# Performance work log

Measured on AMD Instinct MI355X. Metric: run time of the kernel, lower is better.

The kernel has to match this reference:

```python
import jax, jax.numpy as jnp
import numpy as np

S, B, TD = 1024, 2, 138
D, H, Dh, L, F = 1024, 16, 64, 8, 2048
EPS = 1e-5


def setup_inputs() -> dict:
    key = jax.random.key(0)
    ks = jax.random.split(key, 32)
    std = 0.02

    def w(k, shape):
        return (jax.random.normal(k, shape, jnp.float32) * std)

    return {
        'tokens': jax.random.normal(ks[0], (S, B, TD), jnp.float32),
        'Win': w(ks[1], (D, TD)), 'bin_': jnp.zeros((D,), jnp.float32),
        'pos_emb': w(ks[2], (S, D)),
        'Wq': w(ks[3], (L, D, D)), 'bq': jnp.zeros((L, D), jnp.float32),
        'Wk': w(ks[4], (L, D, D)), 'bk': jnp.zeros((L, D), jnp.float32),
        'Wv': w(ks[5], (L, D, D)), 'bv': jnp.zeros((L, D), jnp.float32),
        'Wo': w(ks[6], (L, D, D)), 'bo': jnp.zeros((L, D), jnp.float32),
        'W1': w(ks[7], (L, F, D)), 'b1': jnp.zeros((L, F), jnp.float32),
        'W2': w(ks[8], (L, D, F)), 'b2': jnp.zeros((L, D), jnp.float32),
        'g1': jnp.ones((L, D), jnp.float32), 'be1': jnp.zeros((L, D), jnp.float32),
        'g2': jnp.ones((L, D), jnp.float32), 'be2': jnp.zeros((L, D), jnp.float32),
        'Wh': w(ks[9], (1, D)), 'bh': jnp.zeros((1,), jnp.float32),
    }


def _ln(x, g, b):
    mu = jnp.mean(x, axis=-1, keepdims=True)
    var = jnp.mean(jnp.square(x - mu), axis=-1, keepdims=True)
    return (x - mu) * jax.lax.rsqrt(var + EPS) * g + b


def _rope_tables(seq_len):
    inv_freq = 1.0 / (10000.0 ** (jnp.arange(0, Dh, 2, dtype=jnp.float32) / Dh))
    ang = jnp.arange(seq_len, dtype=jnp.float32)[:, None] * inv_freq  # (S, Dh/2)
    cos = jnp.repeat(jnp.cos(ang), 2, axis=-1)  # (S, Dh) interleaved
    sin = jnp.repeat(jnp.sin(ang), 2, axis=-1)
    return cos, sin


def _apply_rope(x, cos, sin):
    # x: (B, H, S, Dh); rotate_every_two: pairs (x0, x1) -> (-x1, x0)
    rot = jnp.stack([-x[..., 1::2], x[..., 0::2]], axis=-1).reshape(x.shape)
    return x * cos + rot * sin


def reference(tokens, Win, bin_, pos_emb, Wq, bq, Wk, bk, Wv, bv, Wo, bo,
              W1, b1, W2, b2, g1, be1, g2, be2, Wh, bh):
    s = tokens.shape[0]
    x = jnp.einsum('sbt,dt->sbd', tokens, Win) + bin_ + pos_emb[:s, None, :]
    cos, sin = _rope_tables(s)
    causal = jnp.tril(jnp.ones((s, s), dtype=bool))
    scale = 1.0 / np.sqrt(Dh)

    def to_heads(y):  # (S,B,D) -> (B,H,S,Dh)
        return jnp.transpose(y.reshape(s, -1, H, Dh), (1, 2, 0, 3))

    def layer(x, p):
        wq, bq_, wk, bk_, wv, bv_, wo, bo_, w1, b1_, w2, b2_, g1_, be1_, g2_, be2_ = p
        qh = _apply_rope(to_heads(jnp.einsum('sbd,ed->sbe', x, wq) + bq_), cos, sin)
        kh = _apply_rope(to_heads(jnp.einsum('sbd,ed->sbe', x, wk) + bk_), cos, sin)
        vh = to_heads(jnp.einsum('sbd,ed->sbe', x, wv) + bv_)
        scores = jnp.einsum('bhqd,bhkd->bhqk', qh, kh) * scale
        scores = jnp.where(causal, scores, -jnp.inf)
        attn = jax.nn.softmax(scores, axis=-1)
        o = jnp.einsum('bhqk,bhkd->bhqd', attn, vh)  # (B,H,S,Dh)
        o = jnp.transpose(o, (2, 0, 1, 3)).reshape(s, -1, D)
        attn_out = jnp.einsum('sbd,ed->sbe', o, wo) + bo_
        src2 = _ln(x + attn_out, g1_, be1_)
        ff = jnp.einsum('sbf,df->sbd', jax.nn.relu(jnp.einsum('sbd,fd->sbf', src2, w1) + b1_), w2) + b2_
        return _ln(src2 + ff, g2_, be2_), None

    params = (Wq, bq, Wk, bk, Wv, bv, Wo, bo, W1, b1, W2, b2, g1, be1, g2, be2)
    x, _ = jax.lax.scan(layer, x, params)
    return jnp.einsum('sbd,od->sbo', x, Wh) + bh  # (S, B, 1)
```

## Files before the change

### kernel.cpp

```cpp
#include <hip/hip_runtime.h>
#include <hip/hip_bf16.h>

typedef __hip_bfloat16 bf16;
typedef float f32x4 __attribute__((ext_vector_type(4)));
typedef float f32x16 __attribute__((ext_vector_type(16)));
typedef short s16x8 __attribute__((ext_vector_type(8)));
typedef int i32x4 __attribute__((ext_vector_type(4)));

#define S_LEN 1024
#define BATCH 2
#define TDIM 138
#define KPAD 160
#define DMOD 1024
#define NHEAD 16
#define DHEAD 64
#define NLAYER 8
#define FDIM 2048
#define MROWS 2048
static const size_t DD_ = (size_t)DMOD * DMOD;
static const size_t FD_ = (size_t)FDIM * DMOD;

__device__ __forceinline__ void load_lds16(const bf16* g, bf16* l) {
  __builtin_amdgcn_global_load_lds((const __attribute__((address_space(1))) void*)g,
                                   (__attribute__((address_space(3))) void*)l, 16, 0, 0);
}

__device__ __forceinline__ unsigned pack2(float a, float b) {
  unsigned x = __builtin_bit_cast(unsigned short, __float2bfloat16(a));
  unsigned y = __builtin_bit_cast(unsigned short, __float2bfloat16(b));
  return x | (y << 16);
}

__device__ __forceinline__ int chunk_start(int c) {
  return c == 0 ? 0 : (c == 1 ? 32 : (c == 2 ? 56 : 72));
}

__global__ __launch_bounds__(256) void f2b_layer(
    const float4* __restrict__ Wq, const float4* __restrict__ Wk,
    const float4* __restrict__ Wv, const float4* __restrict__ Wo,
    const float4* __restrict__ W1, const float4* __restrict__ W2,
    ushort4* __restrict__ dst) {
  int i = blockIdx.x * 256 + threadIdx.x;
  const int DD4 = (int)(DD_ / 4), FD4 = (int)(FD_ / 4);
  if (i >= 4 * DD4 + 2 * FD4) return;
  const float4* src; int off;
  if (i < 3 * DD4) { int w = i / DD4; off = i - w * DD4; src = w == 0 ? Wq : (w == 1 ? Wk : Wv); }
  else if (i < 4 * DD4) { src = Wo; off = i - 3 * DD4; }
  else if (i < 4 * DD4 + FD4) { src = W1; off = i - 4 * DD4; }
  else { src = W2; off = i - 4 * DD4 - FD4; }
  float4 v = src[off];
  ushort4 o;
  o.x = __builtin_bit_cast(unsigned short, __float2bfloat16(v.x));
  o.y = __builtin_bit_cast(unsigned short, __float2bfloat16(v.y));
  o.z = __builtin_bit_cast(unsigned short, __float2bfloat16(v.z));
  o.w = __builtin_bit_cast(unsigned short, __float2bfloat16(v.w));
  dst[i] = o;
}

__global__ __launch_bounds__(256) void pad_cvt(const float* __restrict__ in,
                                               bf16* __restrict__ out, int R) {
  int i = blockIdx.x * 256 + threadIdx.x;
  if (i >= R * KPAD) return;
  int r = i / KPAD, t = i - r * KPAD;
  out[i] = __float2bfloat16(t < TDIM ? in[r * TDIM + t] : 0.0f);
}

__global__ __launch_bounds__(256) void rope_table(float2* __restrict__ t) {
  int idx = blockIdx.x * 256 + threadIdx.x;
  if (idx >= S_LEN * 32) return;
  int s = idx >> 5, i = idx & 31;
  float freq = __expf(-(float)i * (2.0f / (float)DHEAD) * 9.210340371976184f);
  float sn, cs;
  sincosf((float)s * freq, &sn, &cs);
  t[idx] = make_float2(cs, sn);
}

template<int TN, int EPI>
__global__ __launch_bounds__(512) void gemm128(
    const bf16* __restrict__ A, const bf16* __restrict__ W,
    const float* __restrict__ b0p, const float* __restrict__ b1p, const float* __restrict__ b2p,
    const float2* __restrict__ rope2, float* __restrict__ Cf,
    bf16* __restrict__ Cb0, bf16* __restrict__ Cb1, bf16* __restrict__ Cb2,
    int N, int K, int nbx) {
  constexpr int NJ = TN / 32;
  constexpr int ASZ = 128 * 32, BSZ = TN * 32;
  __shared__ bf16 As[4 * ASZ];
  __shared__ bf16 Bs[4 * BSZ];
  int nwg = gridDim.x, bid = blockIdx.x;
  int wg = (bid & 7) * (nwg >> 3) + (bid >> 3);
  int bx = wg % nbx, by = wg / nbx;
  int bn = bx * TN, bm = by * 128;
  int tid = threadIdx.x, lane = tid & 63, w = tid >> 6;
  int lo = lane & 15, hi = lane >> 4;
  int wr = (w >> 1) * 32, wc = (w & 1) * (TN / 2);
  f32x4 acc[2][NJ] = {};

  int srow = tid >> 2, sseg = tid & 3;
  int srb = (tid & 255) >> 2;
  const bf16* gA = A + (size_t)(bm + srow) * K + sseg * 8;
  const bf16* gB = W + (size_t)(bn + (TN == 128 ? srow : srb)) * K + sseg * 8;
  bf16* lA0 = As + srow * 32 + sseg * 8;
  bf16* lB0 = Bs + (TN == 128 ? srow : srb) * 32 + sseg * 8;

  auto STAGE = [&](int k0, int b) {
    load_lds16(gA + k0, lA0 + b * ASZ);
    if constexpr (TN == 128) {
      load_lds16(gB + k0, lB0 + b * BSZ);
    } else {
      if (tid < 256) load_lds16(gB + k0, lB0 + b * BSZ);
    }
  };

  int nt = K / 32;
  STAGE(0, 0);
  STAGE(32, 1);
  STAGE(64, 2);

  for (int t = 0; t < nt; t++) {
    int rem = nt - 1 - t;
    if constexpr (TN == 128) {
      if (rem >= 2)      asm volatile("s_waitcnt vmcnt(4)" ::: "memory");
      else if (rem == 1) asm volatile("s_waitcnt vmcnt(2)" ::: "memory");
      else               asm volatile("s_waitcnt vmcnt(0)" ::: "memory");
    } else {
      if (tid < 256) {
        if (rem >= 2)      asm volatile("s_waitcnt vmcnt(4)" ::: "memory");
        else if (rem == 1) asm volatile("s_waitcnt vmcnt(2)" ::: "memory");
        else               asm volatile("s_waitcnt vmcnt(0)" ::: "memory");
      } else {
        if (rem >= 2)      asm volatile("s_waitcnt vmcnt(2)" ::: "memory");
        else if (rem == 1) asm volatile("s_waitcnt vmcnt(1)" ::: "memory");
        else               asm volatile("s_waitcnt vmcnt(0)" ::: "memory");
      }
    }
    __builtin_amdgcn_s_barrier();
    __builtin_amdgcn_sched_barrier(0);

    const bf16* Ab = As + (t & 3) * ASZ;
    const bf16* Bb = Bs + (t & 3) * BSZ;
    s16x8 af[2], bfr[NJ];
#pragma unroll
    for (int mi = 0; mi < 2; mi++) af[mi] = *(const s16x8*)(Ab + (wr + mi * 16 + lo) * 32 + hi * 8);
#pragma unroll
    for (int nj = 0; nj < NJ; nj++) bfr[nj] = *(const s16x8*)(Bb + (wc + nj * 16 + lo) * 32 + hi * 8);
#pragma unroll
    for (int mi = 0; mi < 2; mi++)
#pragma unroll
      for (int nj = 0; nj < NJ; nj++)
        acc[mi][nj] = __builtin_amdgcn_mfma_f32_16x16x32_bf16(af[mi], bfr[nj], acc[mi][nj], 0, 0, 0);

    __builtin_amdgcn_sched_barrier(0);
    __builtin_amdgcn_s_barrier();
    __builtin_amdgcn_sched_barrier(0);
    if (t + 3 < nt) STAGE((t + 3) * 32, (t + 3) & 3);
  }

#pragma unroll
  for (int mi = 0; mi < 2; mi++)
#pragma unroll
    for (int nj = 0; nj < NJ; nj++)
#pragma unroll
      for (int r = 0; r < 4; r++) {
        int m = bm + wr + mi * 16 + hi * 4 + r;
        int n = bn + wc + nj * 16 + lo;
        float v = acc[mi][nj][r];
        if constexpr (EPI == 0) {
          int which = n >> 10;
          int d = n & 1023, h = d >> 6, dh = d & 63;
          int s = m >> 1, bb = m & 1;
          const float* bp = which == 0 ? b0p : (which == 1 ? b1p : b2p);
          v += bp[d];
          if (which < 2) {
            float pv = __shfl_xor(v, 1);
            float2 cn = rope2[s * 32 + (dh >> 1)];
            float o = (dh & 1) ? (v * cn.x + pv * cn.y) : (v * cn.x - pv * cn.y);
            bf16* dst = which == 0 ? Cb0 : Cb1;
            dst[(((size_t)(bb * NHEAD + h)) * S_LEN + s) * DHEAD + dh] = __float2bfloat16(o);
          } else {
            Cb2[(((size_t)(bb * NHEAD + h)) * DHEAD + dh) * S_LEN + s] = __float2bfloat16(v);
          }
        } else if constexpr (EPI == 1) {
          Cf[(size_t)m * N + n] = v + b0p[n];
        } else if constexpr (EPI == 2) {
          Cb0[(size_t)m * N + n] = __float2bfloat16(fmaxf(v + b0p[n], 0.0f));
        } else {
          float v2 = v + b0p[n] + b1p[(size_t)(m >> 1) * DMOD + n];
          Cf[(size_t)m * N + n] = v2;
          Cb0[(size_t)m * N + n] = __float2bfloat16(v2);
        }
      }
}

__global__ __launch_bounds__(256) void flash_part(const bf16* __restrict__ Q,
    const bf16* __restrict__ K, const bf16* __restrict__ Vt,
    float* __restrict__ pO, float* __restrict__ pML) {
  int bid = blockIdx.x;
  int xcd = bid & 7, idx = bid >> 3;
  int bh = xcd * 4 + idx / 20;
  int w = threadIdx.x >> 6, lane = threadIdx.x & 63;
  int widx = (idx % 20) * 4 + w;
  int c = widx < 32 ? 0 : (widx < 56 ? 1 : (widx < 72 ? 2 : 3));
  int qt = widx - chunk_start(c) + 8 * c;
  int l31 = lane & 31, hi1 = lane >> 5;
  int q0 = qt * 32, kc0 = c * 256;
  int kend = min(kc0 + 256, q0 + 32);
  int nkt = (kend - kc0 + 31) >> 5;

  const size_t qkb = (size_t)bh * S_LEN * DHEAD;
  const bf16* qp = Q + qkb + (size_t)(q0 + l31) * DHEAD + hi1 * 8;
  s16x8 bq0 = *(const s16x8*)(qp);
  s16x8 bq1 = *(const s16x8*)(qp + 16);
  s16x8 bq2 = *(const s16x8*)(qp + 32);
  s16x8 bq3 = *(const s16x8*)(qp + 48);
  const bf16* kB = K + qkb;
  const bf16* vB = Vt + qkb;
  f32x16 accO0 = {}, accO1 = {};
  float mv = -INFINITY, lv = 0.0f;
  const float SC = 0.18033688011112042f;

  auto loadTile = [&](int kc, s16x8& k0, s16x8& k1, s16x8& k2, s16x8& k3,
                      s16x8& v0, s16x8& v1, s16x8& v2, s16x8& v3) {
    const bf16* kp = kB + (size_t)(kc + l31) * DHEAD + hi1 * 8;
    k0 = *(const s16x8*)(kp);
    k1 = *(const s16x8*)(kp + 16);
    k2 = *(const s16x8*)(kp + 32);
    k3 = *(const s16x8*)(kp + 48);
    const bf16* vp = vB + (size_t)l31 * S_LEN + kc + hi1 * 8;
    v0 = *(const s16x8*)(vp);
    v1 = *(const s16x8*)(vp + 16);
    v2 = *(const s16x8*)(vp + (size_t)32 * S_LEN);
    v3 = *(const s16x8*)(vp + (size_t)32 * S_LEN + 16);
  };

  auto computeTile = [&](int kc, s16x8 ka0, s16x8 ka1, s16x8 ka2, s16x8 ka3,
                         s16x8 va00, s16x8 va01, s16x8 va10, s16x8 va11) {
    f32x16 st = {};
    st = __builtin_amdgcn_mfma_f32_32x32x16_bf16(ka0, bq0, st, 0, 0, 0);
    st = __builtin_amdgcn_mfma_f32_32x32x16_bf16(ka1, bq1, st, 0, 0, 0);
    st = __builtin_amdgcn_mfma_f32_32x32x16_bf16(ka2, bq2, st, 0, 0, 0);
    st = __builtin_amdgcn_mfma_f32_32x32x16_bf16(ka3, bq3, st, 0, 0, 0);

    bool diag = (kc >= q0);
    float pmax = -INFINITY;
#pragma unroll
    for (int j = 0; j < 16; j++) {
      float s = st[j] * SC;
      if (diag) {
        int krow = kc + (j & 3) + 8 * (j >> 2) + 4 * hi1;
        if (krow > q0 + l31) s = -INFINITY;
      }
      st[j] = s;
      pmax = fmaxf(pmax, s);
    }
    pmax = fmaxf(pmax, __shfl_xor(pmax, 32));
    float mnew = fmaxf(mv, pmax);
    float fs = exp2f(mv - mnew);
    float sum = 0.0f;
#pragma unroll
    for (int j = 0; j < 16; j++) {
      float e = exp2f(st[j] - mnew);
      st[j] = e;
      sum += e;
    }
    sum += __shfl_xor(sum, 32);
    lv = lv * fs + sum;
    mv = mnew;
    accO0 = accO0 * fs;
    accO1 = accO1 * fs;

    unsigned w0 = pack2(st[0], st[1]),   w1 = pack2(st[2], st[3]);
    unsigned w2 = pack2(st[4], st[5]),   w3 = pack2(st[6], st[7]);
    unsigned w4 = pack2(st[8], st[9]),   w5 = pack2(st[10], st[11]);
    unsigned w6 = pack2(st[12], st[13]), w7 = pack2(st[14], st[15]);
    unsigned xw0 = (unsigned)__shfl_xor((int)w0, 32), xw1 = (unsigned)__shfl_xor((int)w1, 32);
    unsigned xw2 = (unsigned)__shfl_xor((int)w2, 32), xw3 = (unsigned)__shfl_xor((int)w3, 32);
    unsigned xw4 = (unsigned)__shfl_xor((int)w4, 32), xw5 = (unsigned)__shfl_xor((int)w5, 32);
    unsigned xw6 = (unsigned)__shfl_xor((int)w6, 32), xw7 = (unsigned)__shfl_xor((int)w7, 32);
    bool hb = (hi1 != 0);
    i32x4 f0, f1;
    f0.x = (int)(hb ? xw2 : w0); f0.y = (int)(hb ? xw3 : w1);
    f0.z = (int)(hb ? w2 : xw0); f0.w = (int)(hb ? w3 : xw1);
    f1.x = (int)(hb ? xw6 : w4); f1.y = (int)(hb ? xw7 : w5);
    f1.z = (int)(hb ? w6 : xw4); f1.w = (int)(hb ? w7 : xw5);
    s16x8 pf0 = __builtin_bit_cast(s16x8, f0);
    s16x8 pf1 = __builtin_bit_cast(s16x8, f1);
    accO0 = __builtin_amdgcn_mfma_f32_32x32x16_bf16(va00, pf0, accO0, 0, 0, 0);
    accO0 = __builtin_amdgcn_mfma_f32_32x32x16_bf16(va01, pf1, accO0, 0, 0, 0);
    accO1 = __builtin_amdgcn_mfma_f32_32x32x16_bf16(va10, pf0, accO1, 0, 0, 0);
    accO1 = __builtin_amdgcn_mfma_f32_32x32x16_bf16(va11, pf1, accO1, 0, 0, 0);
  };

  s16x8 A0, A1, A2, A3, A4, A5, A6, A7;
  s16x8 B0, B1, B2, B3, B4, B5, B6, B7;
  loadTile(kc0, A0, A1, A2, A3, A4, A5, A6, A7);
  for (int kt = 0; kt < nkt; kt += 2) {
    if (kt + 1 < nkt) loadTile(kc0 + (kt + 1) * 32, B0, B1, B2, B3, B4, B5, B6, B7);
    computeTile(kc0 + kt * 32, A0, A1, A2, A3, A4, A5, A6, A7);
    if (kt + 1 < nkt) {
      if (kt + 2 < nkt) loadTile(kc0 + (kt + 2) * 32, A0, A1, A2, A3, A4, A5, A6, A7);
      computeTile(kc0 + (kt + 1) * 32, B0, B1, B2, B3, B4, B5, B6, B7);
    }
  }

  int pbase = bh * 80 + widx;
  float* po = pO + (size_t)pbase * 2048 + l31 * 64 + 4 * hi1;
#pragma unroll
  for (int jj = 0; jj < 4; jj++) {
    f32x4 v0 = {accO0[4 * jj], accO0[4 * jj + 1], accO0[4 * jj + 2], accO0[4 * jj + 3]};
    f32x4 v1 = {accO1[4 * jj], accO1[4 * jj + 1], accO1[4 * jj + 2], accO1[4 * jj + 3]};
    *(f32x4*)(po + 8 * jj) = v0;
    *(f32x4*)(po + 32 + 8 * jj) = v1;
  }
  if (hi1 == 0) {
    pML[pbase * 64 + l31] = mv;
    pML[pbase * 64 + 32 + l31] = lv;
  }
}

__global__ __launch_bounds__(256) void flash_merge(const float* __restrict__ pO,
    const float* __restrict__ pML, bf16* __restrict__ O) {
  int bid = blockIdx.x;
  int xcd = bid & 7, idx = bid >> 3;
  int bh = xcd * 4 + idx / 32, qt = idx % 32;
  int b = bh >> 4, h = bh & 15;
  int nch = (qt >> 3) + 1;
  int t = threadIdx.x;
  int dh = t & 63, r0 = t >> 6;
  int ibase = bh * 80;
#pragma unroll
  for (int j = 0; j < 8; j++) {
    int row = j * 4 + r0;
    float ms = -INFINITY;
    for (int cc = 0; cc < nch; cc++) {
      int wi = chunk_start(cc) + qt - 8 * cc;
      ms = fmaxf(ms, pML[(ibase + wi) * 64 + row]);
    }
    float l = 0.0f, o = 0.0f;
    for (int cc = 0; cc < nch; cc++) {
      int wi = chunk_start(cc) + qt - 8 * cc;
      float wgt = exp2f(pML[(ibase + wi) * 64 + row] - ms);
      l += wgt * pML[(ibase + wi) * 64 + 32 + row];
      o += wgt * pO[(size_t)(ibase + wi) * 2048 + row * 64 + dh];
    }
    int q = qt * 32 + row;
    O[((size_t)q * BATCH + b) * DMOD + h * DHEAD + dh] = __float2bfloat16(o / l);
  }
}

__global__ __launch_bounds__(256) void ln_kernel(const float* __restrict__ a,
    const float* __restrict__ r, const float* __restrict__ g,
    const float* __restrict__ be, float* __restrict__ outf, bf16* __restrict__ outb) {
  int m = blockIdx.x;
  int tid = threadIdx.x;
  float vals[4];
  float s1 = 0.f, s2 = 0.f;
  for (int j = 0; j < 4; j++) {
    int d = tid + j * 256;
    float v = a[(size_t)m * DMOD + d] + r[(size_t)m * DMOD + d];
    vals[j] = v; s1 += v; s2 += v * v;
  }
  __shared__ float red[8];
  for (int d = 1; d < 64; d <<= 1) { s1 += __shfl_xor(s1, d); s2 += __shfl_xor(s2, d); }
  int w = tid >> 6, lane = tid & 63;
  if (lane == 0) { red[w] = s1; red[4 + w] = s2; }
  __syncthreads();
  s1 = red[0] + red[1] + red[2] + red[3];
  s2 = red[4] + red[5] + red[6] + red[7];
  float mean = s1 * (1.0f / DMOD);
  float var = s2 * (1.0f / DMOD) - mean * mean;
  float rstd = rsqrtf(var + 1e-5f);
  for (int j = 0; j < 4; j++) {
    int d = tid + j * 256;
    float o = (vals[j] - mean) * rstd * g[d] + be[d];
    outf[(size_t)m * DMOD + d] = o;
    outb[(size_t)m * DMOD + d] = __float2bfloat16(o);
  }
}

__global__ __launch_bounds__(256) void head_kernel(const float* __restrict__ x,
    const float* __restrict__ Wh, const float* __restrict__ bh, float* __restrict__ out) {
  int m = blockIdx.x * 4 + (threadIdx.x >> 6);
  int lane = threadIdx.x & 63;
  float s = 0.f;
  for (int j = 0; j < 16; j++) {
    int d = lane + j * 64;
    s += x[(size_t)m * DMOD + d] * Wh[d];
  }
  for (int d = 1; d < 64; d <<= 1) s += __shfl_xor(s, d);
  if (lane == 0) out[m] = s + bh[0];
}

extern "C" void kernel_launch(void* const* d_in, const int* in_sizes, int n_in,
                              void* d_out, int out_size, void* d_ws, size_t ws_size,
                              hipStream_t stream) {
  (void)in_sizes; (void)n_in; (void)out_size; (void)ws_size;
  const float* tokens = (const float*)d_in[0];
  const float* Win    = (const float*)d_in[1];
  const float* binp   = (const float*)d_in[2];
  const float* pos    = (const float*)d_in[3];
  const float* Wq     = (const float*)d_in[4];
  const float* bq     = (const float*)d_in[5];
  const float* Wk     = (const float*)d_in[6];
  const float* bk     = (const float*)d_in[7];
  const float* Wv     = (const float*)d_in[8];
  const float* bv     = (const float*)d_in[9];
  const float* Wo     = (const float*)d_in[10];
  const float* bo     = (const float*)d_in[11];
  const float* W1     = (const float*)d_in[12];
  const float* b1     = (const float*)d_in[13];
  const float* W2     = (const float*)d_in[14];
  const float* b2     = (const float*)d_in[15];
  const float* g1     = (const float*)d_in[16];
  const float* be1    = (const float*)d_in[17];
  const float* g2     = (const float*)d_in[18];
  const float* be2    = (const float*)d_in[19];
  const float* Wh     = (const float*)d_in[20];
  const float* bhp    = (const float*)d_in[21];
  float* out = (float*)d_out;

  char* p = (char*)d_ws;
  auto alloc = [&](size_t bytes) { char* r = p; p += (bytes + 255) & ~(size_t)255; return r; };
  float* xf   = (float*)alloc((size_t)MROWS * DMOD * 4);
  bf16*  xb   = (bf16*) alloc((size_t)MROWS * DMOD * 2);
  float* x2f  = (float*)alloc((size_t)MROWS * DMOD * 4);
  bf16*  x2b  = (bf16*) alloc((size_t)MROWS * DMOD * 2);
  float* tmpf = (float*)alloc((size_t)MROWS * DMOD * 4);
  bf16*  qb   = (bf16*) alloc((size_t)MROWS * DMOD * 2);
  bf16*  kb   = (bf16*) alloc((size_t)MROWS * DMOD * 2);
  bf16*  vt   = (bf16*) alloc((size_t)MROWS * DMOD * 2);
  bf16*  ob   = (bf16*) alloc((size_t)MROWS * DMOD * 2);
  bf16*  hb   = (bf16*) alloc((size_t)MROWS * FDIM * 2);
  bf16*  wb   = (bf16*) alloc((4 * DD_ + 2 * FD_) * 2);
  bf16*  tokb = (bf16*) alloc((size_t)MROWS * KPAD * 2);
  bf16*  winb = (bf16*) alloc((size_t)DMOD * KPAD * 2);
  float2* rope2 = (float2*)alloc((size_t)S_LEN * 32 * 8);
  float* pO   = (float*)alloc((size_t)32 * 80 * 2048 * 4);
  float* pML  = (float*)alloc((size_t)32 * 80 * 64 * 4);

  rope_table<<<(S_LEN * 32 + 255) / 256, 256, 0, stream>>>(rope2);
  pad_cvt<<<(MROWS * KPAD + 255) / 256, 256, 0, stream>>>(tokens, tokb, MROWS);
  pad_cvt<<<(DMOD * KPAD + 255) / 256, 256, 0, stream>>>(Win, winb, DMOD);
  gemm128<128, 3><<<128, 512, 0, stream>>>(
      tokb, winb, binp, pos, nullptr, nullptr,
      xf, xb, nullptr, nullptr, DMOD, KPAD, 8);

  const int nW4 = (int)((4 * DD_ + 2 * FD_) / 4);

  for (int l = 0; l < NLAYER; l++) {
    f2b_layer<<<(nW4 + 255) / 256, 256, 0, stream>>>(
        (const float4*)(Wq + l * DD_), (const float4*)(Wk + l * DD_),
        (const float4*)(Wv + l * DD_), (const float4*)(Wo + l * DD_),
        (const float4*)(W1 + l * FD_), (const float4*)(W2 + l * FD_), (ushort4*)wb);

    gemm128<128, 0><<<384, 512, 0, stream>>>(
        xb, wb, bq + l * DMOD, bk + l * DMOD, bv + l * DMOD, rope2,
        nullptr, qb, kb, vt, 3 * DMOD, DMOD, 24);

    flash_part<<<640, 256, 0, stream>>>(qb, kb, vt, pO, pML);
    flash_merge<<<1024, 256, 0, stream>>>(pO, pML, ob);

    gemm128<64, 1><<<256, 512, 0, stream>>>(
        ob, wb + 3 * DD_, bo + l * DMOD, nullptr, nullptr, nullptr,
        tmpf, nullptr, nullptr, nullptr, DMOD, DMOD, 16);

    ln_kernel<<<MROWS, 256, 0, stream>>>(xf, tmpf, g1 + l * DMOD, be1 + l * DMOD, x2f, x2b);

    gemm128<128, 2><<<256, 512, 0, stream>>>(
        x2b, wb + 4 * DD_, b1 + l * FDIM, nullptr, nullptr, nullptr,
        nullptr, hb, nullptr, nullptr, FDIM, DMOD, 16);

    gemm128<64, 1><<<256, 512, 0, stream>>>(
        hb, wb + 4 * DD_ + FD_, b2 + l * DMOD, nullptr, nullptr, nullptr,
        tmpf, nullptr, nullptr, nullptr, DMOD, FDIM, 16);

    ln_kernel<<<MROWS, 256, 0, stream>>>(x2f, tmpf, g2 + l * DMOD, be2 + l * DMOD, xf, xb);
  }

  head_kernel<<<MROWS / 4, 256, 0, stream>>>(xf, Wh, bhp, out);
}
```

Before: 1.498 ms.

## Fuse fp32-to-bf16 weight conversion into GEMM B-operand staging

Removes the per-layer f2b_layer kernel and has each GEMM load fp32 weights straight into registers, convert them to bf16 and write them to a double-buffered LDS slot, while A still uses async global-to-LDS loads. It also swaps the tile ordering so consecutive workgroups walk M within an N column, which keeps weight tiles shared in cache. This avoids a separate weight pass and its workspace round trip, at the cost of twice the fp32 weight bytes per tile, register-based loads, conversion ALU work, and an extra lgkmcnt wait inside the pipeline.

```diff
diff --git a/kernel.cpp b/kernel.cpp
--- a/kernel.cpp
+++ b/kernel.cpp
@@ -35,28 +35,6 @@
   return c == 0 ? 0 : (c == 1 ? 32 : (c == 2 ? 56 : 72));
 }
 
-__global__ __launch_bounds__(256) void f2b_layer(
-    const float4* __restrict__ Wq, const float4* __restrict__ Wk,
-    const float4* __restrict__ Wv, const float4* __restrict__ Wo,
-    const float4* __restrict__ W1, const float4* __restrict__ W2,
-    ushort4* __restrict__ dst) {
-  int i = blockIdx.x * 256 + threadIdx.x;
-  const int DD4 = (int)(DD_ / 4), FD4 = (int)(FD_ / 4);
-  if (i >= 4 * DD4 + 2 * FD4) return;
-  const float4* src; int off;
-  if (i < 3 * DD4) { int w = i / DD4; off = i - w * DD4; src = w == 0 ? Wq : (w == 1 ? Wk : Wv); }
-  else if (i < 4 * DD4) { src = Wo; off = i - 3 * DD4; }
-  else if (i < 4 * DD4 + FD4) { src = W1; off = i - 4 * DD4; }
-  else { src = W2; off = i - 4 * DD4 - FD4; }
-  float4 v = src[off];
-  ushort4 o;
-  o.x = __builtin_bit_cast(unsigned short, __float2bfloat16(v.x));
-  o.y = __builtin_bit_cast(unsigned short, __float2bfloat16(v.y));
-  o.z = __builtin_bit_cast(unsigned short, __float2bfloat16(v.z));
-  o.w = __builtin_bit_cast(unsigned short, __float2bfloat16(v.w));
-  dst[i] = o;
-}
-
 __global__ __launch_bounds__(256) void pad_cvt(const float* __restrict__ in,
                                                bf16* __restrict__ out, int R) {
   int i = blockIdx.x * 256 + threadIdx.x;
@@ -75,20 +53,21 @@
   t[idx] = make_float2(cs, sn);
 }
 
-template<int TN, int EPI>
+template<int TN, int EPI, bool BF32>
 __global__ __launch_bounds__(512) void gemm128(
-    const bf16* __restrict__ A, const bf16* __restrict__ W,
+    const bf16* __restrict__ A, const bf16* __restrict__ Wb,
+    const float* __restrict__ Wf0, const float* __restrict__ Wf1, const float* __restrict__ Wf2,
     const float* __restrict__ b0p, const float* __restrict__ b1p, const float* __restrict__ b2p,
     const float2* __restrict__ rope2, float* __restrict__ Cf,
     bf16* __restrict__ Cb0, bf16* __restrict__ Cb1, bf16* __restrict__ Cb2,
-    int N, int K, int nbx) {
+    int N, int K, int nby) {
   constexpr int NJ = TN / 32;
   constexpr int ASZ = 128 * 32, BSZ = TN * 32;
   __shared__ bf16 As[4 * ASZ];
-  __shared__ bf16 Bs[4 * BSZ];
+  __shared__ bf16 Bs[(BF32 ? 2 : 4) * BSZ];
   int nwg = gridDim.x, bid = blockIdx.x;
   int wg = (bid & 7) * (nwg >> 3) + (bid >> 3);
-  int bx = wg % nbx, by = wg / nbx;
+  int by = wg % nby, bx = wg / nby;
   int bn = bx * TN, bm = by * 128;
   int tid = threadIdx.x, lane = tid & 63, w = tid >> 6;
   int lo = lane & 15, hi = lane >> 4;
@@ -96,63 +75,119 @@
   f32x4 acc[2][NJ] = {};
 
   int srow = tid >> 2, sseg = tid & 3;
-  int srb = (tid & 255) >> 2;
   const bf16* gA = A + (size_t)(bm + srow) * K + sseg * 8;
-  const bf16* gB = W + (size_t)(bn + (TN == 128 ? srow : srb)) * K + sseg * 8;
   bf16* lA0 = As + srow * 32 + sseg * 8;
-  bf16* lB0 = Bs + (TN == 128 ? srow : srb) * 32 + sseg * 8;
-
-  auto STAGE = [&](int k0, int b) {
-    load_lds16(gA + k0, lA0 + b * ASZ);
-    if constexpr (TN == 128) {
-      load_lds16(gB + k0, lB0 + b * BSZ);
+
+  const float* WB = nullptr; int bnl = bn;
+  if constexpr (BF32) {
+    if constexpr (EPI == 0) {
+      int wq = bn >> 10;
+      WB = wq == 0 ? Wf0 : (wq == 1 ? Wf1 : Wf2);
+      bnl = bn & 1023;
     } else {
-      if (tid < 256) load_lds16(gB + k0, lB0 + b * BSZ);
-    }
+      WB = Wf0;
+    }
+  }
+  int brow = (TN == 128) ? (tid >> 2) : (tid >> 3);
+  int bcol = (TN == 128) ? ((tid & 3) * 8) : ((tid & 7) * 4);
+  const float* gBf = BF32 ? (WB + (size_t)(bnl + brow) * K + bcol) : nullptr;
+  bf16* lBw = Bs + brow * 32 + bcol;
+  const bf16* gBh = nullptr; bf16* lB0 = nullptr;
+  if constexpr (!BF32) {
+    gBh = Wb + (size_t)(bn + srow) * K + sseg * 8;
+    lB0 = Bs + srow * 32 + sseg * 8;
+  }
+
+  int nt = K / 32;
+
+  auto COMPUTE = [&](int abuf, int bbuf) {
+    const bf16* Ab = As + abuf * ASZ;
+    const bf16* Bb = Bs + bbuf * BSZ;
+    s16x8 af[2], bfr[NJ];
+#pragma unroll
+    for (int mi = 0; mi < 2; mi++) af[mi] = *(const s16x8*)(Ab + (wr + mi * 16 + lo) * 32 + hi * 8);
+#pragma unroll
+    for (int nj = 0; nj < NJ; nj++) bfr[nj] = *(const s16x8*)(Bb + (wc + nj * 16 + lo) * 32 + hi * 8);
+#pragma unroll
+    for (int mi = 0; mi < 2; mi++)
+#pragma unroll
+      for (int nj = 0; nj < NJ; nj++)
+        acc[mi][nj] = __builtin_amdgcn_mfma_f32_16x16x32_bf16(af[mi], bfr[nj], acc[mi][nj], 0, 0, 0);
   };
 
-  int nt = K / 32;
-  STAGE(0, 0);
-  STAGE(32, 1);
-  STAGE(64, 2);
-
-  for (int t = 0; t < nt; t++) {
-    int rem = nt - 1 - t;
-    if constexpr (TN == 128) {
+  if constexpr (BF32) {
+    auto loadB = [&](int k0, f32x4& ra, f32x4& rb) {
+      ra = *(const f32x4*)(gBf + k0);
+      if constexpr (TN == 128) rb = *(const f32x4*)(gBf + k0 + 4);
+    };
+    auto storeB = [&](f32x4 ra, f32x4 rb, int buf) {
+      if constexpr (TN == 128) {
+        union { s16x8 v; unsigned u[4]; } r;
+        r.u[0] = pack2(ra[0], ra[1]); r.u[1] = pack2(ra[2], ra[3]);
+        r.u[2] = pack2(rb[0], rb[1]); r.u[3] = pack2(rb[2], rb[3]);
+        *(s16x8*)(lBw + buf * BSZ) = r.v;
+      } else {
+        union { uint2 v; unsigned u[2]; } r;
+        r.u[0] = pack2(ra[0], ra[1]); r.u[1] = pack2(ra[2], ra[3]);
+        *(uint2*)(lBw + buf * BSZ) = r.v;
+      }
+    };
+    load_lds16(gA, lA0);
+    f32x4 bEa{}, bEb{}, bOa{}, bOb{};
+    loadB(0, bEa, bEb);
+    loadB(32, bOa, bOb);
+    load_lds16(gA + 32, lA0 + ASZ);
+    load_lds16(gA + 64, lA0 + 2 * ASZ);
+
+    for (int t = 0; t < nt; t++) {
+      int rem = nt - 1 - t;
+      if constexpr (TN == 128) {
+        if (t == 0)        asm volatile("s_waitcnt vmcnt(4)" ::: "memory");
+        else if (t == 1)   asm volatile("s_waitcnt vmcnt(5)" ::: "memory");
+        else if (rem >= 2) asm volatile("s_waitcnt vmcnt(4)" ::: "memory");
+        else if (rem == 1) asm volatile("s_waitcnt vmcnt(3)" ::: "memory");
+        else               asm volatile("s_waitcnt vmcnt(0)" ::: "memory");
+      } else {
+        if (t == 0)        asm volatile("s_waitcnt vmcnt(3)" ::: "memory");
+        else if (t == 1)   asm volatile("s_waitcnt vmcnt(4)" ::: "memory");
+        else if (rem >= 2) asm volatile("s_waitcnt vmcnt(3)" ::: "memory");
+        else if (rem == 1) asm volatile("s_waitcnt vmcnt(2)" ::: "memory");
+        else               asm volatile("s_waitcnt vmcnt(0)" ::: "memory");
+      }
+      if ((t & 1) == 0) storeB(bEa, bEb, 0);
+      else              storeB(bOa, bOb, 1);
+      asm volatile("s_waitcnt lgkmcnt(0)" ::: "memory");
+      __builtin_amdgcn_s_barrier();
+      __builtin_amdgcn_sched_barrier(0);
+      COMPUTE(t & 3, t & 1);
+      __builtin_amdgcn_sched_barrier(0);
+      __builtin_amdgcn_s_barrier();
+      __builtin_amdgcn_sched_barrier(0);
+      if (t + 2 < nt) {
+        if ((t & 1) == 0) loadB((t + 2) * 32, bEa, bEb);
+        else              loadB((t + 2) * 32, bOa, bOb);
+      }
+      if (t + 3 < nt) load_lds16(gA + (t + 3) * 32, lA0 + ((t + 3) & 3) * ASZ);
+    }
+  } else {
+    auto STAGE = [&](int k0, int b) {
+      load_lds16(gA + k0, lA0 + b * ASZ);
+      load_lds16(gBh + k0, lB0 + b * BSZ);
+    };
+    STAGE(0, 0); STAGE(32, 1); STAGE(64, 2);
+    for (int t = 0; t < nt; t++) {
+      int rem = nt - 1 - t;
       if (rem >= 2)      asm volatile("s_waitcnt vmcnt(4)" ::: "memory");
       else if (rem == 1) asm volatile("s_waitcnt vmcnt(2)" ::: "memory");
       else               asm volatile("s_waitcnt vmcnt(0)" ::: "memory");
-    } else {
-      if (tid < 256) {
-        if (rem >= 2)      asm volatile("s_waitcnt vmcnt(4)" ::: "memory");
-        else if (rem == 1) asm volatile("s_waitcnt vmcnt(2)" ::: "memory");
-        else               asm volatile("s_waitcnt vmcnt(0)" ::: "memory");
-      } else {
-        if (rem >= 2)      asm volatile("s_waitcnt vmcnt(2)" ::: "memory");
-        else if (rem == 1) asm volatile("s_waitcnt vmcnt(1)" ::: "memory");
-        else               asm volatile("s_waitcnt vmcnt(0)" ::: "memory");
-      }
-    }
-    __builtin_amdgcn_s_barrier();
-    __builtin_amdgcn_sched_barrier(0);
-
-    const bf16* Ab = As + (t & 3) * ASZ;
-    const bf16* Bb = Bs + (t & 3) * BSZ;
-    s16x8 af[2], bfr[NJ];
-#pragma unroll
-    for (int mi = 0; mi < 2; mi++) af[mi] = *(const s16x8*)(Ab + (wr + mi * 16 + lo) * 32 + hi * 8);
-#pragma unroll
-    for (int nj = 0; nj < NJ; nj++) bfr[nj] = *(const s16x8*)(Bb + (wc + nj * 16 + lo) * 32 + hi * 8);
-#pragma unroll
-    for (int mi = 0; mi < 2; mi++)
-#pragma unroll
-      for (int nj = 0; nj < NJ; nj++)
-        acc[mi][nj] = __builtin_amdgcn_mfma_f32_16x16x32_bf16(af[mi], bfr[nj], acc[mi][nj], 0, 0, 0);
-
-    __builtin_amdgcn_sched_barrier(0);
-    __builtin_amdgcn_s_barrier();
-    __builtin_amdgcn_sched_barrier(0);
-    if (t + 3 < nt) STAGE((t + 3) * 32, (t + 3) & 3);
+      __builtin_amdgcn_s_barrier();
+      __builtin_amdgcn_sched_barrier(0);
+      COMPUTE(t & 3, t & 3);
+      __builtin_amdgcn_sched_barrier(0);
+      __builtin_amdgcn_s_barrier();
+      __builtin_amdgcn_sched_barrier(0);
+      if (t + 3 < nt) STAGE((t + 3) * 32, (t + 3) & 3);
+    }
   }
 
 #pragma unroll
@@ -430,7 +465,6 @@
   bf16*  vt   = (bf16*) alloc((size_t)MROWS * DMOD * 2);
   bf16*  ob   = (bf16*) alloc((size_t)MROWS * DMOD * 2);
   bf16*  hb   = (bf16*) alloc((size_t)MROWS * FDIM * 2);
-  bf16*  wb   = (bf16*) alloc((4 * DD_ + 2 * FD_) * 2);
   bf16*  tokb = (bf16*) alloc((size_t)MROWS * KPAD * 2);
   bf16*  winb = (bf16*) alloc((size_t)DMOD * KPAD * 2);
   float2* rope2 = (float2*)alloc((size_t)S_LEN * 32 * 8);
@@ -440,37 +474,35 @@
   rope_table<<<(S_LEN * 32 + 255) / 256, 256, 0, stream>>>(rope2);
   pad_cvt<<<(MROWS * KPAD + 255) / 256, 256, 0, stream>>>(tokens, tokb, MROWS);
   pad_cvt<<<(DMOD * KPAD + 255) / 256, 256, 0, stream>>>(Win, winb, DMOD);
-  gemm128<128, 3><<<128, 512, 0, stream>>>(
-      tokb, winb, binp, pos, nullptr, nullptr,
-      xf, xb, nullptr, nullptr, DMOD, KPAD, 8);
-
-  const int nW4 = (int)((4 * DD_ + 2 * FD_) / 4);
+  gemm128<128, 3, false><<<128, 512, 0, stream>>>(
+      tokb, winb, nullptr, nullptr, nullptr,
+      binp, pos, nullptr, nullptr,
+      xf, xb, nullptr, nullptr, DMOD, KPAD, 16);
 
   for (int l = 0; l < NLAYER; l++) {
-    f2b_layer<<<(nW4 + 255) / 256, 256, 0, stream>>>(
-        (const float4*)(Wq + l * DD_), (const float4*)(Wk + l * DD_),
-        (const float4*)(Wv + l * DD_), (const float4*)(Wo + l * DD_),
-        (const float4*)(W1 + l * FD_), (const float4*)(W2 + l * FD_), (ushort4*)wb);
-
-    gemm128<128, 0><<<384, 512, 0, stream>>>(
-        xb, wb, bq + l * DMOD, bk + l * DMOD, bv + l * DMOD, rope2,
-        nullptr, qb, kb, vt, 3 * DMOD, DMOD, 24);
+    gemm128<128, 0, true><<<384, 512, 0, stream>>>(
+        xb, nullptr, Wq + l * DD_, Wk + l * DD_, Wv + l * DD_,
+        bq + l * DMOD, bk + l * DMOD, bv + l * DMOD, rope2,
+        nullptr, qb, kb, vt, 3 * DMOD, DMOD, 16);
 
     flash_part<<<640, 256, 0, stream>>>(qb, kb, vt, pO, pML);
     flash_merge<<<1024, 256, 0, stream>>>(pO, pML, ob);
 
-    gemm128<64, 1><<<256, 512, 0, stream>>>(
-        ob, wb + 3 * DD_, bo + l * DMOD, nullptr, nullptr, nullptr,
+    gemm128<64, 1, true><<<256, 512, 0, stream>>>(
+        ob, nullptr, Wo + l * DD_, nullptr, nullptr,
+        bo + l * DMOD, nullptr, nullptr, nullptr,
         tmpf, nullptr, nullptr, nullptr, DMOD, DMOD, 16);
 
     ln_kernel<<<MROWS, 256, 0, stream>>>(xf, tmpf, g1 + l * DMOD, be1 + l * DMOD, x2f, x2b);
 
-    gemm128<128, 2><<<256, 512, 0, stream>>>(
-        x2b, wb + 4 * DD_, b1 + l * FDIM, nullptr, nullptr, nullptr,
+    gemm128<128, 2, true><<<256, 512, 0, stream>>>(
+        x2b, nullptr, W1 + l * FD_, nullptr, nullptr,
+        b1 + l * FDIM, nullptr, nullptr, nullptr,
         nullptr, hb, nullptr, nullptr, FDIM, DMOD, 16);
 
-    gemm128<64, 1><<<256, 512, 0, stream>>>(
-        hb, wb + 4 * DD_ + FD_, b2 + l * DMOD, nullptr, nullptr, nullptr,
+    gemm128<64, 1, true><<<256, 512, 0, stream>>>(
+        hb, nullptr, W2 + l * FD_, nullptr, nullptr,
+        b2 + l * DMOD, nullptr, nullptr, nullptr,
         tmpf, nullptr, nullptr, nullptr, DMOD, FDIM, 16);
 
     ln_kernel<<<MROWS, 256, 0, stream>>>(x2f, tmpf, g2 + l * DMOD, be2 + l * DMOD, xf, xb);
```

After: 2.289 ms. +52.8%, slower.
